# Performance work log

Hardware: AMD Instinct MI355X
Metric: run time of the kernel (lower is better)

Reference implementation:

```python
import jax, jax.numpy as jnp
import numpy as np

N_VERBS = 500
N_ROLES = 190
VOCAB = 2000
R = 6            # max_role_count
EMB = 512        # embed_hidden == lstm_hidden
MLP = 1024       # mlp_hidden
C = 512          # conv base size
H = W = 7
NP = H * W
NC = C + 2       # conv channels + 2 coord channels


def _lin(k, fan_in, fan_out):
    kw, kb = jax.random.split(k)
    s = 1.0 / np.sqrt(fan_in)
    return (jax.random.uniform(kw, (fan_in, fan_out), jnp.float32, -s, s),
            jax.random.uniform(kb, (fan_out,), jnp.float32, -s, s))


def setup_inputs() -> dict:
    key = jax.random.key(0)
    ks = jax.random.split(key, 16)
    inp = {}
    inp['conv_feat'] = jax.random.normal(ks[0], (2, C, H, W), jnp.float32)
    inp['verbs'] = jax.random.randint(ks[1], (2,), 0, N_VERBS, jnp.int32)
    inp['roles'] = jax.random.randint(ks[2], (2, R), 0, N_ROLES, jnp.int32)
    inp['verb_emb'] = jax.random.normal(ks[3], (N_VERBS, EMB), jnp.float32)
    inp['role_emb'] = jax.random.normal(ks[4], (N_ROLES + 1, EMB), jnp.float32)
    inp['vW1'], inp['vb1'] = _lin(ks[5], NP * C, MLP)
    inp['vW2'], inp['vb2'] = _lin(ks[6], MLP, MLP)
    inp['vW3'], inp['vb3'] = _lin(ks[7], MLP, N_VERBS)
    inp['gW1'], inp['gb1'] = _lin(ks[8], 2 * NC + EMB, MLP)
    inp['gW2'], inp['gb2'] = _lin(ks[9], MLP, MLP)
    inp['gW3'], inp['gb3'] = _lin(ks[10], MLP, 2 * MLP)
    inp['gW4'], inp['gb4'] = _lin(ks[11], 2 * MLP, 4 * MLP)
    inp['fW1'], inp['fb1'] = _lin(ks[12], 4 * MLP, 4 * MLP)
    inp['fW2'], inp['fb2'] = _lin(ks[13], 4 * MLP, 2 * MLP)
    inp['fW3'], inp['fb3'] = _lin(ks[14], 2 * MLP, VOCAB)
    return inp


def _coords():
    c = jnp.linspace(-4.0, 4.0, H)
    x = jnp.broadcast_to(c[None, :], (H, W))   # x varies along width
    y = jnp.broadcast_to(c[:, None], (H, W))   # y varies along height
    return jnp.stack([x, y]).reshape(2, NP).T  # [NP, 2]


def reference(conv_feat, verbs, roles, verb_emb, role_emb,
              vW1, vb1, vW2, vb2, vW3, vb3,
              gW1, gb1, gW2, gb2, gW3, gb3, gW4, gb4,
              fW1, fb1, fW2, fb2, fW3, fb3):
    relu = jax.nn.relu
    B = conv_feat.shape[0]

    # verb head
    flat = conv_feat.reshape(B, NP * C)
    v = relu(flat @ vW1 + vb1)
    v = relu(v @ vW2 + vb2)
    verb_pred = v @ vW3 + vb3                                  # [B, N_VERBS]

    # role-verb query
    rv = (verb_emb[verbs][:, None, :] * role_emb[roles]).reshape(B * R, EMB)

    # per-role conv features + coord channels -> [Bu, NP, NC]
    feat = jnp.broadcast_to(conv_feat[:, None], (B, R, C, H, W)).reshape(B * R, C, NP)
    feat = jnp.concatenate([feat.transpose(0, 2, 1),
                            jnp.broadcast_to(_coords()[None], (B * R, NP, 2))], axis=2)

    # first g layer: concat([o_j, o_i, qst]) @ gW1 == split matmuls + broadcast add
    Wa, Wb, Wc = gW1[:NC], gW1[NC:2 * NC], gW1[2 * NC:]
    A = feat @ Wa          # pairs with conv1 (index j)
    Bm = feat @ Wb         # pairs with conv2 (index i)
    Q = rv @ Wc
    h = relu(A[:, None, :, :] + Bm[:, :, None, :] + Q[:, None, None, :] + gb1)  # [Bu, NP, NP, MLP]
    h = relu(h @ gW2 + gb2)
    h = relu(h @ gW3 + gb3)
    h = relu(h @ gW4 + gb4)                                    # [Bu, NP, NP, 4*MLP]
    g = h.sum(axis=(1, 2))                                     # [Bu, 4*MLP]

    f = relu(g @ fW1 + fb1)
    f = relu(f @ fW2 + fb2)
    f = f @ fW3 + fb3                                          # [Bu, VOCAB]
    role_predict = f.reshape(B, R, VOCAB)
    return verb_pred, role_predict
```

## Files before the change

### kernel.cpp

```cpp
#include <hip/hip_runtime.h>
#include <cstdint>

typedef _Float16 f16;
typedef f16 f16x8 __attribute__((ext_vector_type(8)));
typedef f16 f16x4 __attribute__((ext_vector_type(4)));
typedef float f32x4 __attribute__((ext_vector_type(4)));

#define GROUP_ROWS 2560
#define VALID_ROWS 2401
#define TPG 10
#define NGROUP 12

template <bool B> struct BoolC { static constexpr bool value = B; };

__device__ __forceinline__ void gll16(const void* g, void* l) {
  __builtin_amdgcn_global_load_lds((const __attribute__((address_space(1))) void*)g,
                                   (__attribute__((address_space(3))) void*)l, 16, 0, 0);
}

__global__ void prep1(const float* __restrict__ gW2, const float* __restrict__ gW3,
                      const float* __restrict__ gW4, f16* __restrict__ W2t,
                      f16* __restrict__ W3t, f16* __restrict__ W4t,
                      const float* __restrict__ conv, const float* __restrict__ gW1,
                      float* __restrict__ abP,
                      const float* __restrict__ verb_emb, const float* __restrict__ role_emb,
                      const int* __restrict__ verbs, const int* __restrict__ roles,
                      float* __restrict__ Qbuf,
                      const float* __restrict__ vW1, float* __restrict__ vp) {
  __shared__ float t[32][33];
  int id = blockIdx.x;
  if (id < 11264) {
    const float* W; f16* Wt; int K, N, local;
    if (id < 1024)      { W = gW2; Wt = W2t; K = 1024; N = 1024; local = id; }
    else if (id < 3072) { W = gW3; Wt = W3t; K = 1024; N = 2048; local = id - 1024; }
    else                { W = gW4; Wt = W4t; K = 2048; N = 4096; local = id - 3072; }
    int ntn = N >> 5;
    int k0 = (local / ntn) * 32, n0 = (local % ntn) * 32;
    int tx = threadIdx.x & 31, ty = threadIdx.x >> 5;
#pragma unroll
    for (int j = 0; j < 4; ++j)
      t[ty + j * 8][tx] = W[(size_t)(k0 + ty + j * 8) * N + n0 + tx];
    __syncthreads();
#pragma unroll
    for (int j = 0; j < 4; ++j)
      Wt[(size_t)(n0 + ty + j * 8) * K + k0 + tx] = (f16)t[tx][ty + j * 8];
  } else if (id < 14400) {
    int local = id - 11264;
    int ky = local / 392, blk = local % 392;
    int nq = blk & 3, bp = blk >> 2;
    int p = bp % 49, b = bp / 49;
    int n = nq * 256 + threadIdx.x;
    int k0 = ky * 66, k1 = k0 + 66;
    if (k1 > 514) k1 = 514;
    float accA = 0.f, accB = 0.f;
    for (int k = k0; k < k1; ++k) {
      float s;
      if (k < 512) s = conv[((size_t)b * 512 + k) * 49 + p];
      else {
        int c7 = (k == 512) ? (p % 7) : (p / 7);
        s = (float)(c7 - 3) * (4.0f / 3.0f);
      }
      accA = fmaf(s, gW1[(size_t)k * 1024 + n], accA);
      accB = fmaf(s, gW1[(size_t)(514 + k) * 1024 + n], accB);
    }
    size_t base = ((size_t)ky * 98 + bp) * 2048;
    abP[base + n] = accA;
    abP[base + 1024 + n] = accB;
  } else if (id < 14448) {
    int local = id - 14400;
    int g = local >> 2, nq = local & 3;
    int b = g / 6;
    int v = verbs[b], ro = roles[g];
    int n = nq * 256 + threadIdx.x;
    const float* ve = verb_emb + (size_t)v * 512;
    const float* re = role_emb + (size_t)ro * 512;
    const float* Wc = gW1 + (size_t)1028 * 1024;
    float acc = 0.f;
#pragma unroll 4
    for (int e = 0; e < 512; ++e)
      acc = fmaf(ve[e] * re[e], Wc[(size_t)e * 1024 + n], acc);
    Qbuf[(size_t)g * 1024 + n] = acc;
  } else {
    int local = id - 14448;
    int nblk = local & 3, kc = local >> 2;
    int n = nblk * 256 + threadIdx.x;
    int k0 = kc * 392, k1 = k0 + 392;
    if (k1 > 25088) k1 = 25088;
    float a0 = 0.f, a1 = 0.f;
#pragma unroll 4
    for (int k = k0; k < k1; ++k) {
      float w = vW1[(size_t)k * 1024 + n];
      a0 = fmaf(conv[k], w, a0);
      a1 = fmaf(conv[25088 + k], w, a1);
    }
    vp[((size_t)kc * 2 + 0) * 1024 + n] = a0;
    vp[((size_t)kc * 2 + 1) * 1024 + n] = a1;
  }
}

__global__ void prep2(const float* __restrict__ abP, float* __restrict__ A,
                      float* __restrict__ Bm, const float* __restrict__ vp,
                      const float* __restrict__ vb1, float* __restrict__ v1b) {
  int id = blockIdx.x;
  if (id < 784) {
    int idx = id * 256 + threadIdx.x;
    if (idx >= 98 * 2048) return;
    int bp = idx >> 11, rem = idx & 2047;
    float s = 0.f;
#pragma unroll
    for (int ky = 0; ky < 8; ++ky) s += abP[((size_t)ky * 98 + bp) * 2048 + rem];
    if (rem < 1024) A[(size_t)bp * 1024 + rem] = s;
    else Bm[(size_t)bp * 1024 + (rem - 1024)] = s;
  } else {
    int idx = (id - 784) * 256 + threadIdx.x;
    int m = idx >> 10, n = idx & 1023;
    float s = vb1[n];
#pragma unroll 4
    for (int kc = 0; kc < 64; ++kc) s += vp[((size_t)kc * 2 + m) * 1024 + n];
    v1b[idx] = s > 0.f ? s : 0.f;
  }
}

__global__ void build_h1(const float* __restrict__ A, const float* __restrict__ Bm,
                         const float* __restrict__ Q, const float* __restrict__ gb1,
                         f16* __restrict__ h1, int g0) {
  int rc = blockIdx.x;
  int gl = rc / GROUP_ROWS;
  int li = rc % GROUP_ROWS;
  int g = g0 + gl;
  int b = g / 6;
  int kk = threadIdx.x * 4;
  f16x4* dst = (f16x4*)(h1 + (size_t)rc * 1024 + kk);
  if (li >= VALID_ROWS) {
    f16x4 z = {(f16)0.f, (f16)0.f, (f16)0.f, (f16)0.f};
    *dst = z;
    return;
  }
  int i = li / 49, j = li % 49;
  const float4 a = *(const float4*)(A + ((size_t)b * 49 + j) * 1024 + kk);
  const float4 bb = *(const float4*)(Bm + ((size_t)b * 49 + i) * 1024 + kk);
  const float4 q = *(const float4*)(Q + (size_t)g * 1024 + kk);
  const float4 bi = *(const float4*)(gb1 + kk);
  float v0 = a.x + bb.x + q.x + bi.x;
  float v1 = a.y + bb.y + q.y + bi.y;
  float v2 = a.z + bb.z + q.z + bi.z;
  float v3 = a.w + bb.w + q.w + bi.w;
  f16x4 r;
  r.x = (f16)(v0 > 0.f ? v0 : 0.f);
  r.y = (f16)(v1 > 0.f ? v1 : 0.f);
  r.z = (f16)(v2 > 0.f ? v2 : 0.f);
  r.w = (f16)(v3 > 0.f ? v3 : 0.f);
  *dst = r;
}

#define WV4 asm volatile("s_waitcnt vmcnt(4)" ::: "memory")
#define WV0 asm volatile("s_waitcnt vmcnt(0)" ::: "memory")

#define LDSA(buf, mf, cc) (*(const f16x8*)(ldsc + (buf)*32768 + arow + (mf)*2048 + (cc)*16))
#define LDSB(buf, nf, cc) (*(const f16x8*)(ldsc + 65536 + (buf)*32768 + brow + (nf)*2048 + (cc)*16))

#define LOADB(BF, buf) { \
  BF[0][0] = LDSB(buf, 0, c0); BF[0][1] = LDSB(buf, 0, c1); \
  BF[1][0] = LDSB(buf, 1, c0); BF[1][1] = LDSB(buf, 1, c1); \
  BF[2][0] = LDSB(buf, 2, c0); BF[2][1] = LDSB(buf, 2, c1); \
  BF[3][0] = LDSB(buf, 3, c0); BF[3][1] = LDSB(buf, 3, c1); }

#define STAGE_A(t, h) { \
  const f16* _g = Aglo + (long)(h) * (128L * K) + (long)(t) * 64; \
  char* _l = ldsc + ((t)&1)*32768 + ((h)*128 + wave*16)*128; \
  gll16(_g, _l); gll16(_g + 8L*K, _l + 1024); }

#define STAGE_B(t, h) { \
  const f16* _g = Bglo + (long)(h) * (128L * K) + (long)(t) * 64; \
  char* _l = ldsc + 65536 + ((t)&1)*32768 + ((h)*128 + wave*16)*128; \
  gll16(_g, _l); gll16(_g + 8L*K, _l + 1024); }

#define PHASE(q, buf, BF, STG, WT, POST) { \
  f16x8 a00 = LDSA(buf, 2*(q), c0);   f16x8 a01 = LDSA(buf, 2*(q), c1); \
  f16x8 a10 = LDSA(buf, 2*(q)+1, c0); f16x8 a11 = LDSA(buf, 2*(q)+1, c1); \
  STG; \
  WT; \
  __builtin_amdgcn_s_barrier(); \
  __builtin_amdgcn_s_setprio(1); \
  _Pragma("unroll") \
  for (int nf = 0; nf < 4; ++nf) { \
    acc[2*(q)][nf]   = __builtin_amdgcn_mfma_f32_16x16x32_f16(a00, BF[nf][0], acc[2*(q)][nf], 0, 0, 0); \
    acc[2*(q)][nf]   = __builtin_amdgcn_mfma_f32_16x16x32_f16(a01, BF[nf][1], acc[2*(q)][nf], 0, 0, 0); \
    acc[2*(q)+1][nf] = __builtin_amdgcn_mfma_f32_16x16x32_f16(a10, BF[nf][0], acc[2*(q)+1][nf], 0, 0, 0); \
    acc[2*(q)+1][nf] = __builtin_amdgcn_mfma_f32_16x16x32_f16(a11, BF[nf][1], acc[2*(q)+1][nf], 0, 0, 0); \
  } \
  __builtin_amdgcn_s_setprio(0); \
  POST; \
  __builtin_amdgcn_s_barrier(); \
}

template <int FUSED>
__global__ __launch_bounds__(512, 2)
void gemm256(const f16* __restrict__ A, const f16* __restrict__ Bt,
             const float* __restrict__ bias, f16* __restrict__ C,
             float* __restrict__ P,
             const float* __restrict__ sx, const float* __restrict__ sw,
             const float* __restrict__ sbias, float* __restrict__ so,
             int sideKind, int gemmN, int N, int K, int ntiles, int aux) {
  __shared__ __align__(16) char ldsbuf[131072];
  char* ldsc = ldsbuf;
  const int tid = threadIdx.x;

  if ((int)blockIdx.x >= gemmN) {
    int sb = blockIdx.x - gemmN;
    int idx = sb * 512 + tid;
    if (sideKind == 2) {
      int m = idx >> 10, n = idx & 1023;
      float s = sbias[n];
#pragma unroll 8
      for (int k = 0; k < 1024; ++k)
        s = fmaf(sx[(size_t)m * 1024 + k], sw[(size_t)k * 1024 + n], s);
      so[idx] = s > 0.f ? s : 0.f;
    } else if (sideKind == 3) {
      if (idx < 1000) {
        int m = idx / 500, n = idx % 500;
        float s = sbias[n];
#pragma unroll 8
        for (int k = 0; k < 1024; ++k)
          s = fmaf(sx[(size_t)m * 1024 + k], sw[(size_t)k * 500 + n], s);
        so[idx] = s;
      }
    }
    return;
  }

  const int wave = tid >> 6, lane = tid & 63;
  const int wm = wave >> 2, wn = wave & 3;
  const int lr = lane & 15, lk = lane >> 4;
  const int c0 = lk ^ (lr & 7), c1 = c0 ^ 4;
  const int arow = (wm * 128 + lr) * 128;
  const int brow = (wn * 64 + lr) * 128;

  int nwg = gemmN, id = blockIdx.x;
  int qq = nwg >> 3, rr8 = nwg & 7;
  int xcd = id & 7, idx = id >> 3;
  int wg = (xcd < rr8 ? xcd * (qq + 1) : rr8 * (qq + 1) + (xcd - rr8) * qq) + idx;
  const int mtile = wg / ntiles, ntile = wg % ntiles;
  const long m0 = (long)mtile * 256, n0 = (long)ntile * 256;

  const int srow = lane >> 3;
  const int schunk = (lane & 7) ^ srow;
  const f16* Aglo = A + (m0 + wave * 16 + srow) * (long)K + schunk * 8;
  const f16* Bglo = Bt + (n0 + wave * 16 + srow) * (long)K + schunk * 8;

  f32x4 acc[8][4] = {};
  f16x8 bFa[4][2], bFb[4][2];

  const int NI = K >> 7;

  STAGE_B(0, 0); STAGE_B(0, 1);
  STAGE_A(0, 0); STAGE_A(0, 1);
  STAGE_B(1, 0); STAGE_B(1, 1);
  WV4;
  __builtin_amdgcn_s_barrier();
  LOADB(bFa, 0);

  auto run_iter = [&](int i, auto lastTag) {
    constexpr bool LAST = decltype(lastTag)::value;
    PHASE(0, 0, bFa, STAGE_A(2*i+1, 0), ;, ;);
    PHASE(1, 0, bFa, STAGE_A(2*i+1, 1), ;, ;);
    PHASE(2, 0, bFa, if constexpr (!LAST) STAGE_B(2*i+2, 0), ;, ;);
    PHASE(3, 0, bFa, if constexpr (!LAST) STAGE_B(2*i+2, 1),
                 if constexpr (LAST) { WV0; } else { WV4; },
                 LOADB(bFb, 1));
    PHASE(0, 1, bFb, if constexpr (!LAST) STAGE_A(2*i+2, 0), ;, ;);
    PHASE(1, 1, bFb, if constexpr (!LAST) STAGE_A(2*i+2, 1), ;, ;);
    PHASE(2, 1, bFb, if constexpr (!LAST) STAGE_B(2*i+3, 0), ;, ;);
    PHASE(3, 1, bFb, if constexpr (!LAST) STAGE_B(2*i+3, 1),
                 if constexpr (!LAST) { WV4; },
                 if constexpr (!LAST) LOADB(bFa, 0));
  };
#pragma unroll 1
  for (int i = 0; i < NI - 1; ++i) run_iter(i, BoolC<false>{});
  run_iter(NI - 1, BoolC<true>{});

  if (FUSED == 0) {
    __syncthreads();
    f16* lt = (f16*)ldsc;
#pragma unroll
    for (int mf = 0; mf < 8; ++mf) {
#pragma unroll
      for (int nf = 0; nf < 4; ++nf) {
        const int col = wn * 64 + nf * 16 + lr;
        const float bv = bias[n0 + col];
#pragma unroll
        for (int r = 0; r < 4; ++r) {
          const int row = wm * 128 + mf * 16 + lk * 4 + r;
          float v = acc[mf][nf][r] + bv;
          v = v > 0.f ? v : 0.f;
          lt[row * 256 + (col ^ (((row >> 2) & 3) << 4))] = (f16)v;
        }
      }
    }
    __syncthreads();
    const int r0 = tid >> 5, ch = tid & 31;
#pragma unroll
    for (int p = 0; p < 16; ++p) {
      const int row = p * 16 + r0;
      const int chs = ch ^ (((row >> 2) & 3) << 1);
      f16x8 v = *(const f16x8*)(lt + row * 256 + chs * 8);
      *(f16x8*)(C + (m0 + row) * N + n0 + ch * 8) = v;
    }
  } else {
    float* csum = (float*)ldsc;
    const int mrel = (mtile % TPG) * 256 + wm * 128;
#pragma unroll
    for (int nf = 0; nf < 4; ++nf) {
      const int col = (int)n0 + wn * 64 + nf * 16 + lr;
      const float bv = bias[col];
      float s = 0.f;
#pragma unroll
      for (int mf = 0; mf < 8; ++mf) {
        const int rb = mrel + mf * 16 + lk * 4;
#pragma unroll
        for (int r = 0; r < 4; ++r) {
          float v = acc[mf][nf][r] + bv;
          v = v > 0.f ? v : 0.f;
          if (rb + r < VALID_ROWS) s += v;
        }
      }
      s += __shfl_xor(s, 16);
      s += __shfl_xor(s, 32);
      if (lk == 0) csum[wm * 256 + wn * 64 + nf * 16 + lr] = s;
    }
    __syncthreads();
    for (int t = tid; t < 256; t += 512)
      P[(long)(aux + mtile) * N + n0 + t] = csum[t] + csum[256 + t];
  }
}

__global__ void reduce_g(const float* __restrict__ P, float* __restrict__ g) {
  int idx = blockIdx.x * 256 + threadIdx.x;
  if (idx >= NGROUP * 4096) return;
  int gi = idx >> 12, n = idx & 4095;
  float s = 0.f;
#pragma unroll
  for (int t = 0; t < TPG; ++t) s += P[(size_t)(gi * TPG + t) * 4096 + n];
  g[idx] = s;
}

__global__ void skinny_part(const float* __restrict__ X, const float* __restrict__ W,
                            float* __restrict__ P, int K, int N, int kchunk) {
  int n = blockIdx.x * 256 + threadIdx.x;
  int k0 = blockIdx.y * kchunk;
  int k1 = k0 + kchunk;
  if (k1 > K) k1 = K;
  if (n >= N) return;
  float acc[12];
#pragma unroll
  for (int m = 0; m < 12; ++m) acc[m] = 0.f;
#pragma unroll 4
  for (int k = k0; k < k1; ++k) {
    float w = W[(size_t)k * N + n];
#pragma unroll
    for (int m = 0; m < 12; ++m) acc[m] = fmaf(X[(size_t)m * K + k], w, acc[m]);
  }
#pragma unroll
  for (int m = 0; m < 12; ++m) P[((size_t)blockIdx.y * 12 + m) * N + n] = acc[m];
}

template <int RELU>
__global__ void skinny_fin(const float* __restrict__ P, const float* __restrict__ bias,
                           float* __restrict__ dst, int N, int KC) {
  int idx = blockIdx.x * 256 + threadIdx.x;
  if (idx >= 12 * N) return;
  int m = idx / N, n = idx - m * N;
  float s = bias ? bias[n] : 0.f;
  for (int kc = 0; kc < KC; ++kc) s += P[((size_t)kc * 12 + m) * N + n];
  if (RELU) s = s > 0.f ? s : 0.f;
  dst[idx] = s;
}

static inline void skinny(const float* X, const float* W, const float* bias, float* dst,
                          float* sp, int K, int N, int relu, hipStream_t stream) {
  int nx = (N + 255) / 256;
  int KC = 1024 / nx;
  if (KC > 256) KC = 256;
  int kmax = K / 16;
  if (kmax < 1) kmax = 1;
  if (KC > kmax) KC = kmax;
  int kchunk = (K + KC - 1) / KC;
  dim3 g1(nx, KC);
  skinny_part<<<g1, 256, 0, stream>>>(X, W, sp, K, N, kchunk);
  int blocks = (12 * N + 255) / 256;
  if (relu)
    skinny_fin<1><<<blocks, 256, 0, stream>>>(sp, bias, dst, N, KC);
  else
    skinny_fin<0><<<blocks, 256, 0, stream>>>(sp, bias, dst, N, KC);
}

extern "C" void kernel_launch(void* const* d_in, const int* in_sizes, int n_in,
                              void* d_out, int out_size, void* d_ws, size_t ws_size,
                              hipStream_t stream) {
  const float* conv = (const float*)d_in[0];
  const int* verbs = (const int*)d_in[1];
  const int* roles = (const int*)d_in[2];
  const float* verb_emb = (const float*)d_in[3];
  const float* role_emb = (const float*)d_in[4];
  const float* vW1 = (const float*)d_in[5];
  const float* vb1 = (const float*)d_in[6];
  const float* vW2 = (const float*)d_in[7];
  const float* vb2 = (const float*)d_in[8];
  const float* vW3 = (const float*)d_in[9];
  const float* vb3 = (const float*)d_in[10];
  const float* gW1 = (const float*)d_in[11];
  const float* gb1 = (const float*)d_in[12];
  const float* gW2 = (const float*)d_in[13];
  const float* gb2 = (const float*)d_in[14];
  const float* gW3 = (const float*)d_in[15];
  const float* gb3 = (const float*)d_in[16];
  const float* gW4 = (const float*)d_in[17];
  const float* gb4 = (const float*)d_in[18];
  const float* fW1 = (const float*)d_in[19];
  const float* fb1 = (const float*)d_in[20];
  const float* fW2 = (const float*)d_in[21];
  const float* fb2 = (const float*)d_in[22];
  const float* fW3 = (const float*)d_in[23];
  const float* fb3 = (const float*)d_in[24];
  float* out = (float*)d_out;

  char* w = (char*)d_ws;
  auto alloc = [&](size_t bytes) {
    char* p = w;
    w += (bytes + 255) & ~(size_t)255;
    return p;
  };
  f16* W2t = (f16*)alloc((size_t)1024 * 1024 * 2);
  f16* W3t = (f16*)alloc((size_t)2048 * 1024 * 2);
  f16* W4t = (f16*)alloc((size_t)4096 * 2048 * 2);
  float* P4 = (float*)alloc((size_t)NGROUP * TPG * 4096 * 4);
  float* Abuf = (float*)alloc((size_t)2 * 49 * 1024 * 4);
  float* Bbuf = (float*)alloc((size_t)2 * 49 * 1024 * 4);
  float* Qbuf = (float*)alloc((size_t)12 * 1024 * 4);
  float* gbuf = (float*)alloc((size_t)12 * 4096 * 4);
  float* sp = (float*)alloc((size_t)128 * 12 * 4096 * 4);
  float* abP = (float*)alloc((size_t)8 * 98 * 2048 * 4);
  float* vp = (float*)alloc((size_t)64 * 2 * 1024 * 4);
  float* f1b = (float*)alloc((size_t)12 * 4096 * 4);
  float* f2b = (float*)alloc((size_t)12 * 2048 * 4);
  float* v1b = (float*)alloc((size_t)2 * 1024 * 4);
  float* v2b = (float*)alloc((size_t)2 * 1024 * 4);

  size_t used = (size_t)(w - (char*)d_ws);
  size_t remain = ws_size > used ? ws_size - used : 0;
  static const int opts[6] = {12, 6, 4, 3, 2, 1};
  int gpc = 1;
  for (int i = 0; i < 6; ++i) {
    size_t need = (size_t)opts[i] * GROUP_ROWS * 4096 * 2 + 4096;
    if (need <= remain) { gpc = opts[i]; break; }
  }
  f16* h1 = (f16*)alloc((size_t)gpc * GROUP_ROWS * 1024 * 2);
  f16* h2 = (f16*)alloc((size_t)gpc * GROUP_ROWS * 1024 * 2);
  f16* h3 = (f16*)alloc((size_t)gpc * GROUP_ROWS * 2048 * 2);
  int nchunks = NGROUP / gpc;

  prep1<<<15472, 256, 0, stream>>>(gW2, gW3, gW4, W2t, W3t, W4t,
                                   conv, gW1, abP,
                                   verb_emb, role_emb, verbs, roles, Qbuf,
                                   vW1, vp);
  prep2<<<792, 256, 0, stream>>>(abP, Abuf, Bbuf, vp, vb1, v1b);

  for (int c = 0; c < nchunks; ++c) {
    int g0 = c * gpc;
    int Mc = gpc * GROUP_ROWS;
    int mt = Mc / 256;
    int s2 = (c == 0) ? 4 : 0, s3 = (c == 0) ? 2 : 0;
    build_h1<<<Mc, 256, 0, stream>>>(Abuf, Bbuf, Qbuf, gb1, h1, g0);
    gemm256<0><<<4 * mt + s2, 512, 0, stream>>>(h1, W2t, gb2, h2, nullptr,
                                                v1b, vW2, vb2, v2b, 2, 4 * mt,
                                                1024, 1024, 4, 0);
    gemm256<0><<<8 * mt + s3, 512, 0, stream>>>(h2, W3t, gb3, h3, nullptr,
                                                v2b, vW3, vb3, out, 3, 8 * mt,
                                                2048, 1024, 8, 0);
    gemm256<1><<<16 * mt, 512, 0, stream>>>(h3, W4t, gb4, nullptr, P4,
                                            nullptr, nullptr, nullptr, nullptr, 0, 16 * mt,
                                            4096, 2048, 16, g0 * TPG);
  }
  reduce_g<<<(NGROUP * 4096 + 255) / 256, 256, 0, stream>>>(P4, gbuf);

  skinny(gbuf, fW1, fb1, f1b, sp, 4096, 4096, 1, stream);
  skinny(f1b, fW2, fb2, f2b, sp, 4096, 2048, 1, stream);
  skinny(f2b, fW3, fb3, out + 1000, sp, 2048, 2000, 0, stream);

  (void)in_sizes; (void)n_in; (void)out_size; (void)ws_size;
}
```

Before: 943.5 us.

## Enlarge GEMM M-tile to 320 rows to reduce padded tiles per group

Changes the main fused GEMM tile from 256x256 to 320x256 rows, so each 2560-row group splits into 8 tiles instead of 10. Each wave now handles 10 m-fragments, staged as 3/3/2/2 per phase, with extra A loads done by half the waves. Single-buffered B fragments and a two-pass epilogue keep register and LDS use within budget. The aim is more MFMA work per LDS B fragment load and fewer blocks, at the cost of larger LDS (144KB), possible occupancy loss and more register pressure.

Result: slower. 1.237 ms (+31.2%).

```diff
diff --git a/kernel.cpp b/kernel.cpp
--- a/kernel.cpp
+++ b/kernel.cpp
@@ -8,7 +8,7 @@
 
 #define GROUP_ROWS 2560
 #define VALID_ROWS 2401
-#define TPG 10
+#define TPG 8
 #define NGROUP 12
 
 template <bool B> struct BoolC { static constexpr bool value = B; };
@@ -156,38 +156,49 @@
 #define WV4 asm volatile("s_waitcnt vmcnt(4)" ::: "memory")
 #define WV0 asm volatile("s_waitcnt vmcnt(0)" ::: "memory")
 
-#define LDSA(buf, mf, cc) (*(const f16x8*)(ldsc + (buf)*32768 + arow + (mf)*2048 + (cc)*16))
-#define LDSB(buf, nf, cc) (*(const f16x8*)(ldsc + 65536 + (buf)*32768 + brow + (nf)*2048 + (cc)*16))
-
-#define LOADB(BF, buf) { \
-  BF[0][0] = LDSB(buf, 0, c0); BF[0][1] = LDSB(buf, 0, c1); \
-  BF[1][0] = LDSB(buf, 1, c0); BF[1][1] = LDSB(buf, 1, c1); \
-  BF[2][0] = LDSB(buf, 2, c0); BF[2][1] = LDSB(buf, 2, c1); \
-  BF[3][0] = LDSB(buf, 3, c0); BF[3][1] = LDSB(buf, 3, c1); }
-
-#define STAGE_A(t, h) { \
-  const f16* _g = Aglo + (long)(h) * (128L * K) + (long)(t) * 64; \
-  char* _l = ldsc + ((t)&1)*32768 + ((h)*128 + wave*16)*128; \
+#define LDSA(buf, mf, cc) (*(const f16x8*)(ldsc + (buf)*40960 + arow + (mf)*2048 + (cc)*16))
+#define LDSB(buf, nf, cc) (*(const f16x8*)(ldsc + 81920 + (buf)*32768 + brow + (nf)*2048 + (cc)*16))
+
+#define LOADB(buf) { \
+  bF[0][0] = LDSB(buf, 0, c0); bF[0][1] = LDSB(buf, 0, c1); \
+  bF[1][0] = LDSB(buf, 1, c0); bF[1][1] = LDSB(buf, 1, c1); \
+  bF[2][0] = LDSB(buf, 2, c0); bF[2][1] = LDSB(buf, 2, c1); \
+  bF[3][0] = LDSB(buf, 3, c0); bF[3][1] = LDSB(buf, 3, c1); }
+
+#define STAGE_A0(t) { \
+  const f16* _g = Aglo + (long)(t) * 64; \
+  char* _l = ldsc + ((t)&1)*40960 + wave*2048; \
   gll16(_g, _l); gll16(_g + 8L*K, _l + 1024); }
+
+#define STAGE_A1(t) { \
+  const f16* _g = Aglo + (long)(t) * 64; \
+  char* _l = ldsc + ((t)&1)*40960 + wave*2048; \
+  gll16(_g + 128L*K, _l + 16384); gll16(_g + 136L*K, _l + 17408); \
+  if (wave < 4) { gll16(_g + 256L*K, _l + 32768); gll16(_g + 264L*K, _l + 33792); } }
 
 #define STAGE_B(t, h) { \
   const f16* _g = Bglo + (long)(h) * (128L * K) + (long)(t) * 64; \
-  char* _l = ldsc + 65536 + ((t)&1)*32768 + ((h)*128 + wave*16)*128; \
+  char* _l = ldsc + 81920 + ((t)&1)*32768 + ((h)*128 + wave*16)*128; \
   gll16(_g, _l); gll16(_g + 8L*K, _l + 1024); }
 
-#define PHASE(q, buf, BF, STG, WT, POST) { \
-  f16x8 a00 = LDSA(buf, 2*(q), c0);   f16x8 a01 = LDSA(buf, 2*(q), c1); \
-  f16x8 a10 = LDSA(buf, 2*(q)+1, c0); f16x8 a11 = LDSA(buf, 2*(q)+1, c1); \
+#define PHASE_MF(buf, MF0, NMF, STG, WT, POST) { \
+  f16x8 aF[3][2]; \
+  _Pragma("unroll") \
+  for (int j = 0; j < (NMF); ++j) { \
+    aF[j][0] = LDSA(buf, (MF0) + j, c0); \
+    aF[j][1] = LDSA(buf, (MF0) + j, c1); \
+  } \
   STG; \
   WT; \
   __builtin_amdgcn_s_barrier(); \
   __builtin_amdgcn_s_setprio(1); \
   _Pragma("unroll") \
-  for (int nf = 0; nf < 4; ++nf) { \
-    acc[2*(q)][nf]   = __builtin_amdgcn_mfma_f32_16x16x32_f16(a00, BF[nf][0], acc[2*(q)][nf], 0, 0, 0); \
-    acc[2*(q)][nf]   = __builtin_amdgcn_mfma_f32_16x16x32_f16(a01, BF[nf][1], acc[2*(q)][nf], 0, 0, 0); \
-    acc[2*(q)+1][nf] = __builtin_amdgcn_mfma_f32_16x16x32_f16(a10, BF[nf][0], acc[2*(q)+1][nf], 0, 0, 0); \
-    acc[2*(q)+1][nf] = __builtin_amdgcn_mfma_f32_16x16x32_f16(a11, BF[nf][1], acc[2*(q)+1][nf], 0, 0, 0); \
+  for (int j = 0; j < (NMF); ++j) { \
+    _Pragma("unroll") \
+    for (int nf = 0; nf < 4; ++nf) { \
+      acc[(MF0)+j][nf] = __builtin_amdgcn_mfma_f32_16x16x32_f16(aF[j][0], bF[nf][0], acc[(MF0)+j][nf], 0, 0, 0); \
+      acc[(MF0)+j][nf] = __builtin_amdgcn_mfma_f32_16x16x32_f16(aF[j][1], bF[nf][1], acc[(MF0)+j][nf], 0, 0, 0); \
+    } \
   } \
   __builtin_amdgcn_s_setprio(0); \
   POST; \
@@ -196,13 +207,13 @@
 
 template <int FUSED>
 __global__ __launch_bounds__(512, 2)
-void gemm256(const f16* __restrict__ A, const f16* __restrict__ Bt,
+void gemm320(const f16* __restrict__ A, const f16* __restrict__ Bt,
              const float* __restrict__ bias, f16* __restrict__ C,
              float* __restrict__ P,
              const float* __restrict__ sx, const float* __restrict__ sw,
              const float* __restrict__ sbias, float* __restrict__ so,
              int sideKind, int gemmN, int N, int K, int ntiles, int aux) {
-  __shared__ __align__(16) char ldsbuf[131072];
+  __shared__ __align__(16) char ldsbuf[147456];
   char* ldsc = ldsbuf;
   const int tid = threadIdx.x;
 
@@ -233,7 +244,7 @@
   const int wm = wave >> 2, wn = wave & 3;
   const int lr = lane & 15, lk = lane >> 4;
   const int c0 = lk ^ (lr & 7), c1 = c0 ^ 4;
-  const int arow = (wm * 128 + lr) * 128;
+  const int arow = (wm * 160 + lr) * 128;
   const int brow = (wn * 64 + lr) * 128;
 
   int nwg = gemmN, id = blockIdx.x;
@@ -241,81 +252,86 @@
   int xcd = id & 7, idx = id >> 3;
   int wg = (xcd < rr8 ? xcd * (qq + 1) : rr8 * (qq + 1) + (xcd - rr8) * qq) + idx;
   const int mtile = wg / ntiles, ntile = wg % ntiles;
-  const long m0 = (long)mtile * 256, n0 = (long)ntile * 256;
+  const long m0 = (long)mtile * 320, n0 = (long)ntile * 256;
 
   const int srow = lane >> 3;
   const int schunk = (lane & 7) ^ srow;
   const f16* Aglo = A + (m0 + wave * 16 + srow) * (long)K + schunk * 8;
   const f16* Bglo = Bt + (n0 + wave * 16 + srow) * (long)K + schunk * 8;
 
-  f32x4 acc[8][4] = {};
-  f16x8 bFa[4][2], bFb[4][2];
+  f32x4 acc[10][4] = {};
+  f16x8 bF[4][2];
 
   const int NI = K >> 7;
 
   STAGE_B(0, 0); STAGE_B(0, 1);
-  STAGE_A(0, 0); STAGE_A(0, 1);
+  STAGE_A0(0); STAGE_A1(0);
   STAGE_B(1, 0); STAGE_B(1, 1);
   WV4;
   __builtin_amdgcn_s_barrier();
-  LOADB(bFa, 0);
+  LOADB(0);
 
   auto run_iter = [&](int i, auto lastTag) {
     constexpr bool LAST = decltype(lastTag)::value;
-    PHASE(0, 0, bFa, STAGE_A(2*i+1, 0), ;, ;);
-    PHASE(1, 0, bFa, STAGE_A(2*i+1, 1), ;, ;);
-    PHASE(2, 0, bFa, if constexpr (!LAST) STAGE_B(2*i+2, 0), ;, ;);
-    PHASE(3, 0, bFa, if constexpr (!LAST) STAGE_B(2*i+2, 1),
-                 if constexpr (LAST) { WV0; } else { WV4; },
-                 LOADB(bFb, 1));
-    PHASE(0, 1, bFb, if constexpr (!LAST) STAGE_A(2*i+2, 0), ;, ;);
-    PHASE(1, 1, bFb, if constexpr (!LAST) STAGE_A(2*i+2, 1), ;, ;);
-    PHASE(2, 1, bFb, if constexpr (!LAST) STAGE_B(2*i+3, 0), ;, ;);
-    PHASE(3, 1, bFb, if constexpr (!LAST) STAGE_B(2*i+3, 1),
-                 if constexpr (!LAST) { WV4; },
-                 if constexpr (!LAST) LOADB(bFa, 0));
+    PHASE_MF(0, 0, 3, STAGE_A0(2*i+1), ;, ;);
+    PHASE_MF(0, 3, 3, STAGE_A1(2*i+1), ;, ;);
+    PHASE_MF(0, 6, 2, if constexpr (!LAST) STAGE_B(2*i+2, 0), ;, ;);
+    PHASE_MF(0, 8, 2, if constexpr (!LAST) STAGE_B(2*i+2, 1),
+             if constexpr (LAST) { WV0; } else { WV4; },
+             LOADB(1));
+    PHASE_MF(1, 0, 3, if constexpr (!LAST) STAGE_A0(2*i+2), ;, ;);
+    PHASE_MF(1, 3, 3, if constexpr (!LAST) STAGE_A1(2*i+2), ;, ;);
+    PHASE_MF(1, 6, 2, if constexpr (!LAST) STAGE_B(2*i+3, 0), ;, ;);
+    PHASE_MF(1, 8, 2, if constexpr (!LAST) STAGE_B(2*i+3, 1),
+             if constexpr (!LAST) { WV4; },
+             if constexpr (!LAST) LOADB(0));
   };
 #pragma unroll 1
   for (int i = 0; i < NI - 1; ++i) run_iter(i, BoolC<false>{});
   run_iter(NI - 1, BoolC<true>{});
 
   if (FUSED == 0) {
-    __syncthreads();
     f16* lt = (f16*)ldsc;
 #pragma unroll
-    for (int mf = 0; mf < 8; ++mf) {
-#pragma unroll
-      for (int nf = 0; nf < 4; ++nf) {
-        const int col = wn * 64 + nf * 16 + lr;
-        const float bv = bias[n0 + col];
-#pragma unroll
-        for (int r = 0; r < 4; ++r) {
-          const int row = wm * 128 + mf * 16 + lk * 4 + r;
-          float v = acc[mf][nf][r] + bv;
-          v = v > 0.f ? v : 0.f;
-          lt[row * 256 + (col ^ (((row >> 2) & 3) << 4))] = (f16)v;
+    for (int half = 0; half < 2; ++half) {
+      __syncthreads();
+      if (wm == half) {
+#pragma unroll
+        for (int mf = 0; mf < 10; ++mf) {
+#pragma unroll
+          for (int nf = 0; nf < 4; ++nf) {
+            const int col = wn * 64 + nf * 16 + lr;
+            const float bv = bias[n0 + col];
+#pragma unroll
+            for (int r = 0; r < 4; ++r) {
+              const int row = mf * 16 + lk * 4 + r;
+              float v = acc[mf][nf][r] + bv;
+              v = v > 0.f ? v : 0.f;
+              lt[row * 256 + (col ^ (((row >> 2) & 3) << 4))] = (f16)v;
+            }
+          }
         }
       }
-    }
-    __syncthreads();
-    const int r0 = tid >> 5, ch = tid & 31;
-#pragma unroll
-    for (int p = 0; p < 16; ++p) {
-      const int row = p * 16 + r0;
-      const int chs = ch ^ (((row >> 2) & 3) << 1);
-      f16x8 v = *(const f16x8*)(lt + row * 256 + chs * 8);
-      *(f16x8*)(C + (m0 + row) * N + n0 + ch * 8) = v;
+      __syncthreads();
+      const int r0 = tid >> 5, ch = tid & 31;
+#pragma unroll
+      for (int p = 0; p < 10; ++p) {
+        const int row = p * 16 + r0;
+        const int chs = ch ^ (((row >> 2) & 3) << 1);
+        f16x8 v = *(const f16x8*)(lt + row * 256 + chs * 8);
+        *(f16x8*)(C + (m0 + half * 160 + row) * N + n0 + ch * 8) = v;
+      }
     }
   } else {
     float* csum = (float*)ldsc;
-    const int mrel = (mtile % TPG) * 256 + wm * 128;
+    const int mrel = (mtile & 7) * 320 + wm * 160;
 #pragma unroll
     for (int nf = 0; nf < 4; ++nf) {
       const int col = (int)n0 + wn * 64 + nf * 16 + lr;
       const float bv = bias[col];
       float s = 0.f;
 #pragma unroll
-      for (int mf = 0; mf < 8; ++mf) {
+      for (int mf = 0; mf < 10; ++mf) {
         const int rb = mrel + mf * 16 + lk * 4;
 #pragma unroll
         for (int r = 0; r < 4; ++r) {
@@ -468,16 +484,16 @@
   for (int c = 0; c < nchunks; ++c) {
     int g0 = c * gpc;
     int Mc = gpc * GROUP_ROWS;
-    int mt = Mc / 256;
+    int mt = Mc / 320;
     int s2 = (c == 0) ? 4 : 0, s3 = (c == 0) ? 2 : 0;
     build_h1<<<Mc, 256, 0, stream>>>(Abuf, Bbuf, Qbuf, gb1, h1, g0);
-    gemm256<0><<<4 * mt + s2, 512, 0, stream>>>(h1, W2t, gb2, h2, nullptr,
+    gemm320<0><<<4 * mt + s2, 512, 0, stream>>>(h1, W2t, gb2, h2, nullptr,
                                                 v1b, vW2, vb2, v2b, 2, 4 * mt,
                                                 1024, 1024, 4, 0);
-    gemm256<0><<<8 * mt + s3, 512, 0, stream>>>(h2, W3t, gb3, h3, nullptr,
+    gemm320<0><<<8 * mt + s3, 512, 0, stream>>>(h2, W3t, gb3, h3, nullptr,
                                                 v2b, vW3, vb3, out, 3, 8 * mt,
                                                 2048, 1024, 8, 0);
-    gemm256<1><<<16 * mt, 512, 0, stream>>>(h3, W4t, gb4, nullptr, P4,
+    gemm320<1><<<16 * mt, 512, 0, stream>>>(h3, W4t, gb4, nullptr, P4,
                                             nullptr, nullptr, nullptr, nullptr, 0, 16 * mt,
                                             4096, 2048, 16, g0 * TPG);
   }
```
